# Performance work log

Measured on AMD Instinct MI355X. Metric: run time of the kernel, lower is better.

## Reference

```python
import jax, jax.numpy as jnp
import numpy as np

B, S, D, H = 4, 2048, 1024, 16
DK = D // H  # 64
THETA = 10000.0


def _rope(x, pos):
    # x: [..., s, d], pos: [s] int. Rotation-matrix RoPE applied to consecutive pairs.
    d = x.shape[-1]
    inv_freq = 1.0 / (THETA ** (jnp.arange(0, d, 2, dtype=jnp.float32) / d))  # [d/2]
    freqs = pos.astype(jnp.float32)[:, None] * inv_freq[None, :]             # [s, d/2]
    cos, sin = jnp.cos(freqs), jnp.sin(freqs)
    xr = x.reshape(x.shape[:-1] + (d // 2, 2))
    x0, x1 = xr[..., 0], xr[..., 1]
    y0 = cos * x0 - sin * x1
    y1 = sin * x0 + cos * x1
    return jnp.stack([y0, y1], axis=-1).reshape(x.shape)


def setup_inputs() -> dict:
    key = jax.random.key(0)
    ks = jax.random.split(key, 5)
    std = float(np.sqrt(2.0 / (D + D)))
    return {
        "x": jax.random.normal(ks[0], (B, S, D), dtype=jnp.float32),
        "token_positions": jnp.arange(S, dtype=jnp.int32),
        "wq": jax.random.normal(ks[1], (D, D), dtype=jnp.float32) * std,
        "wk": jax.random.normal(ks[2], (D, D), dtype=jnp.float32) * std,
        "wv": jax.random.normal(ks[3], (D, D), dtype=jnp.float32) * std,
        "wo": jax.random.normal(ks[4], (D, D), dtype=jnp.float32) * std,
    }


def reference(x, token_positions, wq, wk, wv, wo):
    # Linear layers use weight [out, in]: y = x @ W^T
    q = jnp.einsum('bsd,od->bso', x, wq).reshape(B, S, H, DK).transpose(0, 2, 1, 3)  # [b,h,s,dk]
    k = jnp.einsum('bsd,od->bso', x, wk).reshape(B, S, H, DK).transpose(0, 2, 1, 3)
    v = jnp.einsum('bsd,od->bso', x, wv).reshape(B, S, H, DK).transpose(0, 2, 1, 3)
    q = _rope(q, token_positions)
    k = _rope(k, token_positions)
    scores = jnp.einsum('bhqd,bhkd->bhqk', q, k) / jnp.sqrt(jnp.float32(DK))
    causal = jnp.tril(jnp.ones((S, S), dtype=bool))
    scores = jnp.where(causal, scores, jnp.finfo(scores.dtype).min)
    attn = jax.nn.softmax(scores, axis=-1)
    o = jnp.einsum('bhqk,bhkd->bhqd', attn, v)          # [b,h,s,dk]
    o = o.transpose(0, 2, 1, 3).reshape(B, S, D)        # [b,s,h*dk]
    return jnp.einsum('bsd,od->bso', o, wo)
```

## Files before the change

### kernel.cpp

```cpp
#include <hip/hip_runtime.h>
#include <hip/hip_bf16.h>
#include <stdint.h>

#define S_LEN 2048
#define NHEAD 16
#define BATCH 4

typedef __attribute__((ext_vector_type(8))) short short8;
typedef __attribute__((ext_vector_type(4))) float f32x4;
typedef __attribute__((ext_vector_type(4))) unsigned short u16x4;
typedef __attribute__((ext_vector_type(2))) unsigned short u16x2;

__device__ __forceinline__ unsigned short f2bf(float f) {
  union { float f; uint32_t u; } a; a.f = f;
  uint32_t r = (a.u + 0x7fff + ((a.u >> 16) & 1)) >> 16;
  return (unsigned short)r;
}
__device__ __forceinline__ float bf2f(unsigned short u) {
  union { uint32_t u; float f; } a; a.u = ((uint32_t)u) << 16;
  return a.f;
}
__device__ __forceinline__ uint32_t pk2bf(float a, float b) {
  union { __hip_bfloat162 h; uint32_t u; } cv;
  cv.h = __float22bfloat162_rn(float2{a, b});
  return cv.u;
}

__device__ __forceinline__ void gload16(const void* g, void* l) {
  __builtin_amdgcn_global_load_lds(
      (const __attribute__((address_space(1))) void*)g,
      (__attribute__((address_space(3))) void*)l, 16, 0, 0);
}

__global__ void k_cvt(const float* __restrict__ src, unsigned short* __restrict__ dst, int n4) {
  int i = blockIdx.x * blockDim.x + threadIdx.x;
  if (i < n4) {
    float4 v = ((const float4*)src)[i];
    union { uint32_t u[2]; u16x4 v; } o;
    o.u[0] = pk2bf(v.x, v.y);
    o.u[1] = pk2bf(v.z, v.w);
    ((u16x4*)dst)[i] = o.v;
  }
}

__global__ void k_cvt4(const float* __restrict__ s0, const float* __restrict__ s1,
                       const float* __restrict__ s2, const float* __restrict__ s3,
                       unsigned short* __restrict__ dst) {
  int i = blockIdx.x * 256 + threadIdx.x;
  int r = i >> 18;
  const float* s = r == 0 ? s0 : r == 1 ? s1 : r == 2 ? s2 : s3;
  float4 v = ((const float4*)s)[i & 0x3FFFF];
  union { uint32_t u[2]; u16x4 v; } o;
  o.u[0] = pk2bf(v.x, v.y);
  o.u[1] = pk2bf(v.z, v.w);
  ((u16x4*)dst)[i] = o.v;
}

template<int OUTF32>
__global__ __launch_bounds__(256) void k_gemm_nt(
    const unsigned short* __restrict__ A, const unsigned short* __restrict__ B,
    void* __restrict__ Cp, int K, int ldc, int gx)
{
  __shared__ unsigned short lA[128 * 64];
  __shared__ unsigned short lB[128 * 64];
  const int tid = threadIdx.x;
  const int w = tid >> 6, lane = tid & 63;
  const int wm = w >> 1, wn = w & 1;
  const int l15 = lane & 15, lg = lane >> 4;
  const int nwg = (int)gridDim.x, slot = (int)blockIdx.x;
  const int f = (slot & 7) * (nwg >> 3) + (slot >> 3);
  const int row0 = (f / gx) * 128, col0 = (f % gx) * 128;

  f32x4 acc[4][4] = {};
  const size_t rsb = (size_t)K * 2;

  for (int k0 = 0; k0 < K; k0 += 64) {
#pragma unroll
    for (int it = 0; it < 4; ++it) {
      int fb = w * 4096 + it * 1024 + lane * 16;
      int r = fb >> 7, cb = fb & 127;
      gload16((const char*)A + (size_t)(row0 + r) * rsb + k0 * 2 + cb,
              (char*)lA + (w * 4096 + it * 1024));
      gload16((const char*)B + (size_t)(col0 + r) * rsb + k0 * 2 + cb,
              (char*)lB + (w * 4096 + it * 1024));
    }
    __syncthreads();
#pragma unroll
    for (int ks = 0; ks < 2; ++ks) {
      short8 af[4], bg[4];
#pragma unroll
      for (int i = 0; i < 4; ++i) {
        int rowa = wm * 64 + i * 16 + l15;
        af[i] = *(const short8*)((const char*)lA + rowa * 128 + ks * 64 + lg * 16);
        int rowb = wn * 64 + i * 16 + l15;
        bg[i] = *(const short8*)((const char*)lB + rowb * 128 + ks * 64 + lg * 16);
      }
#pragma unroll
      for (int i = 0; i < 4; ++i)
#pragma unroll
        for (int j = 0; j < 4; ++j)
          acc[i][j] = __builtin_amdgcn_mfma_f32_16x16x32_bf16(af[i], bg[j], acc[i][j], 0, 0, 0);
    }
    __syncthreads();
  }

#pragma unroll
  for (int i = 0; i < 4; ++i)
#pragma unroll
    for (int j = 0; j < 4; ++j)
#pragma unroll
      for (int r = 0; r < 4; ++r) {
        int row = row0 + wm * 64 + i * 16 + lg * 4 + r;
        int col = col0 + wn * 64 + j * 16 + l15;
        float v = acc[i][j][r];
        if (OUTF32) ((float*)Cp)[(size_t)row * ldc + col] = v;
        else ((unsigned short*)Cp)[(size_t)row * ldc + col] = f2bf(v);
      }
}

__global__ void k_tab(const int* __restrict__ pos, float* __restrict__ tab) {
  int i = blockIdx.x * 256 + threadIdx.x;
  int s = i >> 5, p = i & 31;
  float fp = (float)pos[s];
  float inv = exp2f(-(float)p * 0.41524101186092029f);
  float ang = fp * inv;
  float sn, cs;
  __sincosf(ang, &sn, &cs);
  const float SCL = 0.18033688011112042f;
  ((float2*)tab)[i] = float2{cs * SCL, sn * SCL};
  ((float2*)tab)[65536 + i] = float2{cs, sn};
}

__global__ void k_rope(unsigned short* __restrict__ qkv, const float* __restrict__ tab) {
  int idx = blockIdx.x * 256 + threadIdx.x;
  int row = idx >> 8;
  int rem = idx & 255;
  int which = rem >> 7;
  int cq = rem & 127;
  int p0 = (cq * 4) & 31;
  int s = row & (S_LEN - 1);
  const float4* tb = (const float4*)(tab + ((which << 17) + (s * 32 + p0) * 2));
  float4 t0 = tb[0], t1 = tb[1];
  size_t off = (size_t)row * 3072 + which * 1024 + cq * 8;
  short8 v = *(short8*)(qkv + off);
  float x0 = bf2f((unsigned short)v[0]), x1 = bf2f((unsigned short)v[1]);
  float x2 = bf2f((unsigned short)v[2]), x3 = bf2f((unsigned short)v[3]);
  float x4 = bf2f((unsigned short)v[4]), x5 = bf2f((unsigned short)v[5]);
  float x6 = bf2f((unsigned short)v[6]), x7 = bf2f((unsigned short)v[7]);
  union { uint32_t u[4]; short8 v; } o;
  o.u[0] = pk2bf(t0.x * x0 - t0.y * x1, t0.y * x0 + t0.x * x1);
  o.u[1] = pk2bf(t0.z * x2 - t0.w * x3, t0.w * x2 + t0.z * x3);
  o.u[2] = pk2bf(t1.x * x4 - t1.y * x5, t1.y * x4 + t1.x * x5);
  o.u[3] = pk2bf(t1.z * x6 - t1.w * x7, t1.w * x6 + t1.z * x7);
  *(short8*)(qkv + off) = o.v;
}

__global__ __launch_bounds__(512) void k_attn(const unsigned short* __restrict__ qkv,
                                              unsigned short* __restrict__ O) {
  __shared__ unsigned short lK[2][64 * 64];
  __shared__ uint32_t lV32[2][64 * 36];

  const int tid = threadIdx.x, w = tid >> 6, lane = tid & 63;
  const int l15 = lane & 15, lg = lane >> 4;
  const int slot = (int)blockIdx.x;
  const int f0 = (slot & 7) * 64 + (slot >> 3);
  const int bh = f0 >> 3, qp = f0 & 7;
  const int b = bh >> 4, h = bh & 15;
  const size_t rstride = 3072;

  short8 vr;

  auto stageK = [&](int buf, int t) {
    int fb = tid * 16;
    int r = fb >> 7;
    int cb = (fb ^ ((r & 7) << 4)) & 127;
    gload16((const char*)qkv + ((size_t)(b * S_LEN + t * 64 + r) * rstride + 1024 + h * 64) * 2 + cb,
            (char*)(&lK[buf][0]) + fb);
  };
  auto loadV = [&](int t) {
    int kp = tid >> 4, sub = tid & 15;
    int pp = sub & 1, c = (sub >> 1) * 8;
    vr = *(const short8*)(qkv + (size_t)(b * S_LEN + t * 64 + kp * 2 + pp) * rstride + 2048 + h * 64 + c);
  };
  auto writeV = [&](int buf) {
    int kp = tid >> 4, sub = tid & 15;
    int pp = sub & 1, c = (sub >> 1) * 8;
    uint32_t u0 = __shfl_xor(((const uint32_t*)&vr)[0], 1);
    uint32_t u1 = __shfl_xor(((const uint32_t*)&vr)[1], 1);
    uint32_t u2 = __shfl_xor(((const uint32_t*)&vr)[2], 1);
    uint32_t u3 = __shfl_xor(((const uint32_t*)&vr)[3], 1);
    unsigned short ov[8];
    ((uint32_t*)ov)[0] = u0; ((uint32_t*)ov)[1] = u1;
    ((uint32_t*)ov)[2] = u2; ((uint32_t*)ov)[3] = u3;
    const unsigned short* own = (const unsigned short*)&vr;
    int colk = ((kp >> 4) << 4) | (((kp >> 1) & 3) << 2) | (((kp >> 3) & 1) << 1) | (kp & 1);
#pragma unroll
    for (int j = 0; j < 4; ++j) {
      int d = c + (pp ? 4 : 0) + j;
      unsigned short lo = pp ? ov[4 + j] : own[j];
      unsigned short hi = pp ? own[4 + j] : ov[j];
      uint32_t packed = (uint32_t)lo | ((uint32_t)hi << 16);
      int colS = colk ^ (((d >> 3) & 7) << 2);
      lV32[buf][d * 36 + colS] = packed;
    }
  };

  for (int seg = 0; seg < 2; ++seg) {
    const int qb = (seg == 0 ? (15 - qp) : qp) * 128;
    const int ntiles = (qb >> 6) + 2;

    short8 qf[2];
    {
      int qrow = qb + w * 16 + l15;
      const unsigned short* qpt = qkv + (size_t)(b * S_LEN + qrow) * rstride + h * 64 + lg * 8;
      qf[0] = *(const short8*)qpt;
      qf[1] = *(const short8*)(qpt + 32);
    }

    float mrun = -3e38f, lrun = 0.f;
    f32x4 oacc[4] = {};

    stageK(0, 0);
    loadV(0);
    writeV(0);
    __syncthreads();

    for (int t = 0; t < ntiles; ++t) {
      const int cur = t & 1, nxt = cur ^ 1;
      const bool more = (t + 1 < ntiles);
      if (more) { stageK(nxt, t + 1); loadV(t + 1); }

      f32x4 sf[4] = {};
      __builtin_amdgcn_s_setprio(1);
#pragma unroll
      for (int ks = 0; ks < 2; ++ks) {
#pragma unroll
        for (int jf = 0; jf < 4; ++jf) {
          int krow = jf * 16 + l15;
          int g = krow * 128 + ks * 64 + lg * 16;
          int a = g ^ ((krow & 7) << 4);
          short8 kb = *(const short8*)((const char*)(&lK[cur][0]) + a);
          sf[jf] = __builtin_amdgcn_mfma_f32_16x16x32_bf16(kb, qf[ks], sf[jf], 0, 0, 0);
        }
      }
      __builtin_amdgcn_s_setprio(0);

      const int kv = t * 64;
      const bool dg = (kv + 63 > qb + w * 16);
      const int qglob = qb + w * 16 + l15;
      float pv[4][4];
      float mx = -3e38f;
#pragma unroll
      for (int jf = 0; jf < 4; ++jf)
#pragma unroll
        for (int r = 0; r < 4; ++r) {
          float v = sf[jf][r];
          if (dg) {
            int kglob = kv + jf * 16 + lg * 4 + r;
            if (kglob > qglob) v = -3e38f;
          }
          pv[jf][r] = v;
          mx = fmaxf(mx, v);
        }
      mx = fmaxf(mx, __shfl_xor(mx, 16));
      mx = fmaxf(mx, __shfl_xor(mx, 32));
      if (!__all(mx - mrun <= 8.0f)) {
        float mn = fmaxf(mrun, mx);
        float alpha = exp2f(mrun - mn);
        mrun = mn;
#pragma unroll
        for (int j = 0; j < 4; ++j)
#pragma unroll
          for (int r = 0; r < 4; ++r)
            oacc[j][r] *= alpha;
        lrun *= alpha;
      }
      float ps = 0.f;
#pragma unroll
      for (int jf = 0; jf < 4; ++jf)
#pragma unroll
        for (int r = 0; r < 4; ++r) {
          float e = exp2f(pv[jf][r] - mrun);
          pv[jf][r] = e;
          ps += e;
        }
      ps += __shfl_xor(ps, 16);
      ps += __shfl_xor(ps, 32);
      lrun += ps;

      __builtin_amdgcn_s_setprio(1);
#pragma unroll
      for (int ks = 0; ks < 2; ++ks) {
        union { uint32_t u[4]; short8 v; } pb;
        pb.u[0] = pk2bf(pv[2 * ks][0], pv[2 * ks][1]);
        pb.u[1] = pk2bf(pv[2 * ks][2], pv[2 * ks][3]);
        pb.u[2] = pk2bf(pv[2 * ks + 1][0], pv[2 * ks + 1][1]);
        pb.u[3] = pk2bf(pv[2 * ks + 1][2], pv[2 * ks + 1][3]);
#pragma unroll
        for (int j = 0; j < 4; ++j) {
          int d = j * 16 + l15;
          int colS = (ks * 16 + lg * 4) ^ (((d >> 3) & 7) << 2);
          short8 vb = *(const short8*)(&lV32[cur][d * 36 + colS]);
          oacc[j] = __builtin_amdgcn_mfma_f32_16x16x32_bf16(vb, pb.v, oacc[j], 0, 0, 0);
        }
      }
      __builtin_amdgcn_s_setprio(0);

      if (more) writeV(nxt);
      __syncthreads();
    }

    float rinv = __builtin_amdgcn_rcpf(lrun);
    int qrow = qb + w * 16 + l15;
    unsigned short* orow = O + (size_t)(b * S_LEN + qrow) * 1024 + h * 64;
#pragma unroll
    for (int j = 0; j < 4; ++j) {
      union { uint32_t u[2]; u16x4 v; } ow;
      ow.u[0] = pk2bf(oacc[j][0] * rinv, oacc[j][1] * rinv);
      ow.u[1] = pk2bf(oacc[j][2] * rinv, oacc[j][3] * rinv);
      *(u16x4*)(orow + j * 16 + lg * 4) = ow.v;
    }
  }
}

extern "C" void kernel_launch(void* const* d_in, const int* in_sizes, int n_in,
                              void* d_out, int out_size, void* d_ws, size_t ws_size,
                              hipStream_t stream) {
  const float* x  = (const float*)d_in[0];
  const int* pos  = (const int*)d_in[1];
  const float* wq = (const float*)d_in[2];
  const float* wk = (const float*)d_in[3];
  const float* wv = (const float*)d_in[4];
  const float* wo = (const float*)d_in[5];
  float* out = (float*)d_out;

  char* ws = (char*)d_ws;
  unsigned short* xb   = (unsigned short*)(ws);
  unsigned short* wqkv = (unsigned short*)(ws + (size_t)16 * 1024 * 1024);
  unsigned short* wob  = (unsigned short*)(ws + (size_t)22 * 1024 * 1024);
  unsigned short* qkv  = (unsigned short*)(ws + (size_t)24 * 1024 * 1024);
  unsigned short* ob   = (unsigned short*)(ws + (size_t)72 * 1024 * 1024);
  float* tab = (float*)xb;

  k_cvt<<<8192, 256, 0, stream>>>(x, xb, 8192 * 1024 / 4);
  k_cvt4<<<4096, 256, 0, stream>>>(wq, wk, wv, wo, wqkv);

  k_gemm_nt<0><<<1536, 256, 0, stream>>>(xb, wqkv, qkv, 1024, 3072, 24);

  k_tab<<<256, 256, 0, stream>>>(pos, tab);
  k_rope<<<8192, 256, 0, stream>>>(qkv, tab);

  k_attn<<<512, 512, 0, stream>>>(qkv, ob);

  k_gemm_nt<1><<<512, 256, 0, stream>>>(ob, wob, out, 1024, 1024, 8);
}
```

Baseline: 310.3 us.

## Fuse RoPE into QKV GEMM epilogue, merge prep kernels, lazy softmax max

Merges the x/weight conversion and RoPE table kernels into one prep launch and applies RoPE in the QKV GEMM epilogue using a lane shuffle, removing the separate RoPE pass over qkv. In attention, the per-tile running max is replaced by a max taken on the first tile plus a fixed-step rescale when sums grow large. Row sums are computed with an extra MFMA against a ones vector instead of shuffles. This cuts launches, memory traffic and per-tile reductions, but risks exp overflow or precision loss if later scores far exceed the first tile's max.

```diff
diff --git a/kernel.cpp b/kernel.cpp
--- a/kernel.cpp
+++ b/kernel.cpp
@@ -9,17 +9,14 @@
 typedef __attribute__((ext_vector_type(8))) short short8;
 typedef __attribute__((ext_vector_type(4))) float f32x4;
 typedef __attribute__((ext_vector_type(4))) unsigned short u16x4;
-typedef __attribute__((ext_vector_type(2))) unsigned short u16x2;
+
+__device__ float2 g_tab[131072];
 
 __device__ __forceinline__ unsigned short f2bf(float f) {
   union { float f; uint32_t u; } a; a.f = f;
   uint32_t r = (a.u + 0x7fff + ((a.u >> 16) & 1)) >> 16;
   return (unsigned short)r;
 }
-__device__ __forceinline__ float bf2f(unsigned short u) {
-  union { uint32_t u; float f; } a; a.u = ((uint32_t)u) << 16;
-  return a.f;
-}
 __device__ __forceinline__ uint32_t pk2bf(float a, float b) {
   union { __hip_bfloat162 h; uint32_t u; } cv;
   cv.h = __float22bfloat162_rn(float2{a, b});
@@ -32,31 +29,41 @@
       (__attribute__((address_space(3))) void*)l, 16, 0, 0);
 }
 
-__global__ void k_cvt(const float* __restrict__ src, unsigned short* __restrict__ dst, int n4) {
-  int i = blockIdx.x * blockDim.x + threadIdx.x;
-  if (i < n4) {
-    float4 v = ((const float4*)src)[i];
+__global__ void k_prep(const float* __restrict__ x, const float* __restrict__ wq,
+                       const float* __restrict__ wk, const float* __restrict__ wv,
+                       const float* __restrict__ wo, const int* __restrict__ pos,
+                       unsigned short* __restrict__ xb, unsigned short* __restrict__ wdst) {
+  int bid = blockIdx.x;
+  if (bid < 8192) {
+    int i = bid * 256 + threadIdx.x;
+    float4 v = ((const float4*)x)[i];
     union { uint32_t u[2]; u16x4 v; } o;
     o.u[0] = pk2bf(v.x, v.y);
     o.u[1] = pk2bf(v.z, v.w);
-    ((u16x4*)dst)[i] = o.v;
+    ((u16x4*)xb)[i] = o.v;
+  } else if (bid < 12288) {
+    int i = (bid - 8192) * 256 + threadIdx.x;
+    int r = i >> 18;
+    const float* s = r == 0 ? wq : r == 1 ? wk : r == 2 ? wv : wo;
+    float4 v = ((const float4*)s)[i & 0x3FFFF];
+    union { uint32_t u[2]; u16x4 v; } o;
+    o.u[0] = pk2bf(v.x, v.y);
+    o.u[1] = pk2bf(v.z, v.w);
+    ((u16x4*)wdst)[i] = o.v;
+  } else {
+    int i = (bid - 12288) * 256 + threadIdx.x;
+    int s = i >> 5, p = i & 31;
+    float fp = (float)pos[s];
+    float inv = exp2f(-(float)p * 0.41524101186092029f);
+    float sn, cs;
+    __sincosf(fp * inv, &sn, &cs);
+    const float SCL = 0.18033688011112042f;
+    g_tab[i] = float2{cs * SCL, sn * SCL};
+    g_tab[65536 + i] = float2{cs, sn};
   }
 }
 
-__global__ void k_cvt4(const float* __restrict__ s0, const float* __restrict__ s1,
-                       const float* __restrict__ s2, const float* __restrict__ s3,
-                       unsigned short* __restrict__ dst) {
-  int i = blockIdx.x * 256 + threadIdx.x;
-  int r = i >> 18;
-  const float* s = r == 0 ? s0 : r == 1 ? s1 : r == 2 ? s2 : s3;
-  float4 v = ((const float4*)s)[i & 0x3FFFF];
-  union { uint32_t u[2]; u16x4 v; } o;
-  o.u[0] = pk2bf(v.x, v.y);
-  o.u[1] = pk2bf(v.z, v.w);
-  ((u16x4*)dst)[i] = o.v;
-}
-
-template<int OUTF32>
+template<int OUTF32, int ROPE>
 __global__ __launch_bounds__(256) void k_gemm_nt(
     const unsigned short* __restrict__ A, const unsigned short* __restrict__ B,
     void* __restrict__ Cp, int K, int ldc, int gx)
@@ -107,52 +114,24 @@
 #pragma unroll
   for (int i = 0; i < 4; ++i)
 #pragma unroll
-    for (int j = 0; j < 4; ++j)
+    for (int j = 0; j < 4; ++j) {
+      int col = col0 + wn * 64 + j * 16 + l15;
 #pragma unroll
       for (int r = 0; r < 4; ++r) {
         int row = row0 + wm * 64 + i * 16 + lg * 4 + r;
-        int col = col0 + wn * 64 + j * 16 + l15;
         float v = acc[i][j][r];
+        if (ROPE) {
+          float vp = __shfl_xor(v, 1);
+          int which = col >> 10;
+          if (which < 2) {
+            float2 t = g_tab[(which << 16) + ((row & (S_LEN - 1)) << 5) + ((col >> 1) & 31)];
+            v = (col & 1) ? (t.y * vp + t.x * v) : (t.x * v - t.y * vp);
+          }
+        }
         if (OUTF32) ((float*)Cp)[(size_t)row * ldc + col] = v;
         else ((unsigned short*)Cp)[(size_t)row * ldc + col] = f2bf(v);
       }
-}
-
-__global__ void k_tab(const int* __restrict__ pos, float* __restrict__ tab) {
-  int i = blockIdx.x * 256 + threadIdx.x;
-  int s = i >> 5, p = i & 31;
-  float fp = (float)pos[s];
-  float inv = exp2f(-(float)p * 0.41524101186092029f);
-  float ang = fp * inv;
-  float sn, cs;
-  __sincosf(ang, &sn, &cs);
-  const float SCL = 0.18033688011112042f;
-  ((float2*)tab)[i] = float2{cs * SCL, sn * SCL};
-  ((float2*)tab)[65536 + i] = float2{cs, sn};
-}
-
-__global__ void k_rope(unsigned short* __restrict__ qkv, const float* __restrict__ tab) {
-  int idx = blockIdx.x * 256 + threadIdx.x;
-  int row = idx >> 8;
-  int rem = idx & 255;
-  int which = rem >> 7;
-  int cq = rem & 127;
-  int p0 = (cq * 4) & 31;
-  int s = row & (S_LEN - 1);
-  const float4* tb = (const float4*)(tab + ((which << 17) + (s * 32 + p0) * 2));
-  float4 t0 = tb[0], t1 = tb[1];
-  size_t off = (size_t)row * 3072 + which * 1024 + cq * 8;
-  short8 v = *(short8*)(qkv + off);
-  float x0 = bf2f((unsigned short)v[0]), x1 = bf2f((unsigned short)v[1]);
-  float x2 = bf2f((unsigned short)v[2]), x3 = bf2f((unsigned short)v[3]);
-  float x4 = bf2f((unsigned short)v[4]), x5 = bf2f((unsigned short)v[5]);
-  float x6 = bf2f((unsigned short)v[6]), x7 = bf2f((unsigned short)v[7]);
-  union { uint32_t u[4]; short8 v; } o;
-  o.u[0] = pk2bf(t0.x * x0 - t0.y * x1, t0.y * x0 + t0.x * x1);
-  o.u[1] = pk2bf(t0.z * x2 - t0.w * x3, t0.w * x2 + t0.z * x3);
-  o.u[2] = pk2bf(t1.x * x4 - t1.y * x5, t1.y * x4 + t1.x * x5);
-  o.u[3] = pk2bf(t1.z * x6 - t1.w * x7, t1.w * x6 + t1.z * x7);
-  *(short8*)(qkv + off) = o.v;
+    }
 }
 
 __global__ __launch_bounds__(512) void k_attn(const unsigned short* __restrict__ qkv,
@@ -205,6 +184,10 @@
     }
   };
 
+  short8 ones;
+#pragma unroll
+  for (int e = 0; e < 8; ++e) ones[e] = (short)0x3F80;
+
   for (int seg = 0; seg < 2; ++seg) {
     const int qb = (seg == 0 ? (15 - qp) : qp) * 128;
     const int ntiles = (qb >> 6) + 2;
@@ -217,8 +200,9 @@
       qf[1] = *(const short8*)(qpt + 32);
     }
 
-    float mrun = -3e38f, lrun = 0.f;
+    float mrun = 0.f;
     f32x4 oacc[4] = {};
+    f32x4 csum = {};
 
     stageK(0, 0);
     loadV(0);
@@ -249,7 +233,6 @@
       const bool dg = (kv + 63 > qb + w * 16);
       const int qglob = qb + w * 16 + l15;
       float pv[4][4];
-      float mx = -3e38f;
 #pragma unroll
       for (int jf = 0; jf < 4; ++jf)
 #pragma unroll
@@ -260,33 +243,22 @@
             if (kglob > qglob) v = -3e38f;
           }
           pv[jf][r] = v;
-          mx = fmaxf(mx, v);
         }
-      mx = fmaxf(mx, __shfl_xor(mx, 16));
-      mx = fmaxf(mx, __shfl_xor(mx, 32));
-      if (!__all(mx - mrun <= 8.0f)) {
-        float mn = fmaxf(mrun, mx);
-        float alpha = exp2f(mrun - mn);
-        mrun = mn;
-#pragma unroll
-        for (int j = 0; j < 4; ++j)
-#pragma unroll
-          for (int r = 0; r < 4; ++r)
-            oacc[j][r] *= alpha;
-        lrun *= alpha;
-      }
-      float ps = 0.f;
+      if (t == 0) {
+        float mx = -3e38f;
+#pragma unroll
+        for (int jf = 0; jf < 4; ++jf)
+#pragma unroll
+          for (int r = 0; r < 4; ++r) mx = fmaxf(mx, pv[jf][r]);
+        mx = fmaxf(mx, __shfl_xor(mx, 16));
+        mx = fmaxf(mx, __shfl_xor(mx, 32));
+        mrun = mx;
+      }
 #pragma unroll
       for (int jf = 0; jf < 4; ++jf)
 #pragma unroll
-        for (int r = 0; r < 4; ++r) {
-          float e = exp2f(pv[jf][r] - mrun);
-          pv[jf][r] = e;
-          ps += e;
-        }
-      ps += __shfl_xor(ps, 16);
-      ps += __shfl_xor(ps, 32);
-      lrun += ps;
+        for (int r = 0; r < 4; ++r)
+          pv[jf][r] = exp2f(pv[jf][r] - mrun);
 
       __builtin_amdgcn_s_setprio(1);
 #pragma unroll
@@ -303,14 +275,26 @@
           short8 vb = *(const short8*)(&lV32[cur][d * 36 + colS]);
           oacc[j] = __builtin_amdgcn_mfma_f32_16x16x32_bf16(vb, pb.v, oacc[j], 0, 0, 0);
         }
+        csum = __builtin_amdgcn_mfma_f32_16x16x32_bf16(ones, pb.v, csum, 0, 0, 0);
       }
       __builtin_amdgcn_s_setprio(0);
 
       if (more) writeV(nxt);
       __syncthreads();
-    }
-
-    float rinv = __builtin_amdgcn_rcpf(lrun);
+
+      if (!__all(csum[0] <= 1.0e9f)) {
+        const float al = 0x1p-32f;
+#pragma unroll
+        for (int j = 0; j < 4; ++j)
+#pragma unroll
+          for (int r = 0; r < 4; ++r) oacc[j][r] *= al;
+#pragma unroll
+        for (int r = 0; r < 4; ++r) csum[r] *= al;
+        mrun += 32.0f;
+      }
+    }
+
+    float rinv = __builtin_amdgcn_rcpf(csum[0]);
     int qrow = qb + w * 16 + l15;
     unsigned short* orow = O + (size_t)(b * S_LEN + qrow) * 1024 + h * 64;
 #pragma unroll
@@ -340,17 +324,12 @@
   unsigned short* wob  = (unsigned short*)(ws + (size_t)22 * 1024 * 1024);
   unsigned short* qkv  = (unsigned short*)(ws + (size_t)24 * 1024 * 1024);
   unsigned short* ob   = (unsigned short*)(ws + (size_t)72 * 1024 * 1024);
-  float* tab = (float*)xb;
-
-  k_cvt<<<8192, 256, 0, stream>>>(x, xb, 8192 * 1024 / 4);
-  k_cvt4<<<4096, 256, 0, stream>>>(wq, wk, wv, wo, wqkv);
-
-  k_gemm_nt<0><<<1536, 256, 0, stream>>>(xb, wqkv, qkv, 1024, 3072, 24);
-
-  k_tab<<<256, 256, 0, stream>>>(pos, tab);
-  k_rope<<<8192, 256, 0, stream>>>(qkv, tab);
+
+  k_prep<<<12544, 256, 0, stream>>>(x, wq, wk, wv, wo, pos, xb, wqkv);
+
+  k_gemm_nt<0, 1><<<1536, 256, 0, stream>>>(xb, wqkv, qkv, 1024, 3072, 24);
 
   k_attn<<<512, 512, 0, stream>>>(qkv, ob);
 
-  k_gemm_nt<1><<<512, 256, 0, stream>>>(ob, wob, out, 1024, 1024, 8);
-}
+  k_gemm_nt<1, 0><<<512, 256, 0, stream>>>(ob, wob, out, 1024, 1024, 8);
+}
```

New measurement: 328.7 us. 5.9% more time.
